# Optimization experiments

Measured on AMD Instinct MI355X. Metric: run time of the kernel, lower is better.

## Reference

```python
import jax, jax.numpy as jnp
import numpy as np

PRUNE_N = 2  # entries zeroed per group
PRUNE_M = 4  # group size along feature dim


def _prune_2of4(x_flat):
    # x_flat: [N, D]; zero out the PRUNE_N smallest-|.| entries in every
    # contiguous group of PRUNE_M columns (matches torch topk(largest=False)
    # + scatter mask semantics, deterministic sort-order tie-breaking).
    N, D = x_flat.shape
    g = x_flat.reshape(N, D // PRUNE_M, PRUNE_M)           # [N, G, 4]
    a = jnp.abs(g)
    order = jnp.argsort(a, axis=-1)                         # ascending |.|
    rank = jnp.argsort(order, axis=-1)                      # rank of each slot
    keep = rank >= PRUNE_N                                  # keep 2 largest
    return jnp.where(keep, g, jnp.zeros_like(g)).reshape(N, D)


def setup_inputs() -> dict:
    key = jax.random.key(0)
    k1, k2 = jax.random.split(key)
    B, S, D_IN, D_OUT = 2, 4096, 4096, 4096
    x = jax.random.normal(k1, (B, S, D_IN), dtype=jnp.float32)
    weight = jax.random.normal(k2, (D_OUT, D_IN), dtype=jnp.float32) * 0.02
    return {"x": x, "weight": weight}


def reference(x, weight):
    B, S, D = x.shape
    x_flat = x.reshape(B * S, D)
    x_sp = _prune_2of4(x_flat)                              # [B*S, D]
    out = x_sp @ weight.T                                   # [B*S, D_out]
    return out
```

## Files before the change

### kernel.cpp

```cpp
#include <hip/hip_runtime.h>
#include <hip/hip_bf16.h>

typedef float f32x4 __attribute__((ext_vector_type(4)));
typedef __bf16 bf16x8 __attribute__((ext_vector_type(8)));
typedef unsigned short ushort_t;
typedef ushort_t u16x8 __attribute__((ext_vector_type(8)));

__device__ inline ushort_t f2bf_rne(float f) {
  unsigned u = __builtin_bit_cast(unsigned, f);
  unsigned r = (u + 0x7fffu + ((u >> 16) & 1u)) >> 16;
  return (ushort_t)r;
}

__global__ void prune_cast_kernel(const float* __restrict__ x,
                                  ushort_t* __restrict__ xsp, long n8) {
  long i = (long)blockIdx.x * blockDim.x + threadIdx.x;
  if (i >= n8) return;
  const float4* p = reinterpret_cast<const float4*>(x);
  float4 g0 = p[2 * i];
  float4 g1 = p[2 * i + 1];
  float v[8] = {g0.x, g0.y, g0.z, g0.w, g1.x, g1.y, g1.z, g1.w};
  u16x8 o;
#pragma unroll
  for (int g = 0; g < 2; ++g) {
    float a[4];
#pragma unroll
    for (int j = 0; j < 4; ++j) a[j] = fabsf(v[g * 4 + j]);
#pragma unroll
    for (int j = 0; j < 4; ++j) {
      int rank = 0;
#pragma unroll
      for (int k = 0; k < 4; ++k) {
        if (k == j) continue;
        rank += (a[k] < a[j]) || (a[k] == a[j] && k < j);
      }
      o[g * 4 + j] = (rank >= 2) ? f2bf_rne(v[g * 4 + j]) : (ushort_t)0;
    }
  }
  reinterpret_cast<u16x8*>(xsp)[i] = o;
}

__global__ void cast_bf16_kernel(const float* __restrict__ w,
                                 ushort_t* __restrict__ wb, long n8) {
  long i = (long)blockIdx.x * blockDim.x + threadIdx.x;
  if (i >= n8) return;
  const float4* p = reinterpret_cast<const float4*>(w);
  float4 g0 = p[2 * i];
  float4 g1 = p[2 * i + 1];
  u16x8 o;
  o[0] = f2bf_rne(g0.x); o[1] = f2bf_rne(g0.y);
  o[2] = f2bf_rne(g0.z); o[3] = f2bf_rne(g0.w);
  o[4] = f2bf_rne(g1.x); o[5] = f2bf_rne(g1.y);
  o[6] = f2bf_rne(g1.z); o[7] = f2bf_rne(g1.w);
  reinterpret_cast<u16x8*>(wb)[i] = o;
}

#define BAR() __builtin_amdgcn_s_barrier()
#define WAIT_LGKM0() asm volatile("s_waitcnt lgkmcnt(0)" ::: "memory")
#define WAIT_VM4() asm volatile("s_waitcnt vmcnt(4)" ::: "memory")

#define STAGE_A(t1, h, par)                                                    \
  {                                                                            \
    const ushort_t* g0 =                                                       \
        A + (a_row0 + (h) * 128 + srow) * (long)Kd + (t1) * 64 + scol;         \
    const ushort_t* g1 =                                                       \
        A + (a_row0 + (h) * 128 + srow + 8) * (long)Kd + (t1) * 64 + scol;     \
    ushort_t* l0 = &ldsA[((par) * 2 + (h)) * 8192 + w * 1024];                 \
    __builtin_amdgcn_global_load_lds(                                          \
        (const __attribute__((address_space(1))) void*)g0,                     \
        (__attribute__((address_space(3))) void*)l0, 16, 0, 0);                \
    __builtin_amdgcn_global_load_lds(                                          \
        (const __attribute__((address_space(1))) void*)g1,                     \
        (__attribute__((address_space(3))) void*)(l0 + 512), 16, 0, 0);        \
  }

#define STAGE_B(t1, h, par)                                                    \
  {                                                                            \
    const ushort_t* g0 =                                                       \
        B + (b_row0 + (h) * 128 + srow) * (long)Kd + (t1) * 64 + scol;         \
    const ushort_t* g1 =                                                       \
        B + (b_row0 + (h) * 128 + srow + 8) * (long)Kd + (t1) * 64 + scol;     \
    ushort_t* l0 = &ldsB[((par) * 2 + (h)) * 8192 + w * 1024];                 \
    __builtin_amdgcn_global_load_lds(                                          \
        (const __attribute__((address_space(1))) void*)g0,                     \
        (__attribute__((address_space(3))) void*)l0, 16, 0, 0);                \
    __builtin_amdgcn_global_load_lds(                                          \
        (const __attribute__((address_space(1))) void*)g1,                     \
        (__attribute__((address_space(3))) void*)(l0 + 512), 16, 0, 0);        \
  }

#define LDA_FRAG(dst, par, mi, s)                                              \
  dst = *reinterpret_cast<const bf16x8*>(                                      \
      reinterpret_cast<const char*>(ldsA) + ((par) * 2 + wr) * 16384 +         \
      (mi) * 2048 + ((s) ? roff1 : roff0));

#define LDB_FRAG(dst, par, ni, s)                                              \
  dst = *reinterpret_cast<const bf16x8*>(                                      \
      reinterpret_cast<const char*>(ldsB) + ((par) * 2 + (wc >> 1)) * 16384 +  \
      (wc & 1) * 8192 + (ni) * 2048 + ((s) ? roff1 : roff0));

#define MFMA_Q(MH, NH)                                                         \
  __builtin_amdgcn_s_setprio(1);                                               \
  _Pragma("unroll") for (int s = 0; s < 2; ++s)                                \
  _Pragma("unroll") for (int mi = 0; mi < 4; ++mi)                             \
  _Pragma("unroll") for (int ni = 0; ni < 2; ++ni)                             \
      acc[(MH) * 4 + mi][(NH) * 2 + ni] =                                      \
          __builtin_amdgcn_mfma_f32_16x16x32_bf16(                             \
              af[mi][s], bfr[(NH) * 2 + ni][s],                                \
              acc[(MH) * 4 + mi][(NH) * 2 + ni], 0, 0, 0);                     \
  __builtin_amdgcn_s_setprio(0);

#define KTILE(t, PAR)                                                          \
  {           \
    _Pragma("unroll") for (int mi = 0; mi < 4; ++mi)                           \
    _Pragma("unroll") for (int s = 0; s < 2; ++s)                              \
        LDA_FRAG(af[mi][s], PAR, mi, s)                                        \
    _Pragma("unroll") for (int ni = 0; ni < 2; ++ni)                           \
    _Pragma("unroll") for (int s = 0; s < 2; ++s)                              \
        LDB_FRAG(bfr[ni][s], PAR, ni, s)                                       \
    if ((t) + 1 < NT) STAGE_A((t) + 1, 0, (PAR) ^ 1)                           \
    BAR();                                                                     \
    WAIT_LGKM0();                                                              \
    MFMA_Q(0, 0)                                                               \
    BAR();                                                                     \
                      \
    _Pragma("unroll") for (int ni = 2; ni < 4; ++ni)                           \
    _Pragma("unroll") for (int s = 0; s < 2; ++s)                              \
        LDB_FRAG(bfr[ni][s], PAR, ni, s)                                       \
    if ((t) + 1 < NT) STAGE_A((t) + 1, 1, (PAR) ^ 1)                           \
    BAR();                                                                     \
    WAIT_LGKM0();                                                              \
    MFMA_Q(0, 1)                                                               \
    BAR();                                                                     \
                        \
    _Pragma("unroll") for (int mi = 0; mi < 4; ++mi)                           \
    _Pragma("unroll") for (int s = 0; s < 2; ++s)                              \
        LDA_FRAG(af[mi][s], PAR, 4 + mi, s)                                    \
    if ((t) + 2 < NT) STAGE_B((t) + 2, 0, PAR)                                 \
    BAR();                                                                     \
    WAIT_LGKM0();                                                              \
    MFMA_Q(1, 1)                                                               \
    BAR();                                                                     \
                 \
    if ((t) + 2 < NT) STAGE_B((t) + 2, 1, PAR)                                 \
    BAR();                                                                     \
    MFMA_Q(1, 0)                                                               \
    WAIT_VM4();                                                                \
    BAR();                                                                     \
  }

__global__ __launch_bounds__(512, 1) void gemm256_kernel(
    const ushort_t* __restrict__ A,
    const ushort_t* __restrict__ B,
    float* __restrict__ C,
    int M, int N, int Kd) {
  __shared__ ushort_t ldsA[4 * 8192];
  __shared__ ushort_t ldsB[4 * 8192];

  const int tid = threadIdx.x;
  const int lane = tid & 63;
  const int w = tid >> 6;
  const int wr = w >> 2;
  const int wc = w & 3;

  const int b = blockIdx.x;
  const int wg = (b & 7) * (gridDim.x >> 3) + (b >> 3);
  const int nbn = N / 256;
  const int bm = wg / nbn, bn = wg % nbn;
  const long a_row0 = (long)bm * 256;
  const long b_row0 = (long)bn * 256;
  const int NT = Kd / 64;

  const int srow = w * 16 + (lane >> 3);
  const int scol = (((lane & 7) ^ ((lane >> 3) & 7)) << 3);

  const int rl = lane & 15;
  const int q = lane >> 4;
  const int roff0 = rl * 128 + (((q) ^ (rl & 7)) << 4);
  const int roff1 = rl * 128 + (((q | 4) ^ (rl & 7)) << 4);

  f32x4 acc[8][4];
#pragma unroll
  for (int i = 0; i < 8; ++i)
#pragma unroll
    for (int j = 0; j < 4; ++j) acc[i][j] = f32x4{0.f, 0.f, 0.f, 0.f};

  bf16x8 af[4][2];
  bf16x8 bfr[4][2];

  STAGE_B(0, 0, 0)
  STAGE_B(0, 1, 0)
  STAGE_A(0, 0, 0)
  STAGE_A(0, 1, 0)
  STAGE_B(1, 0, 1)
  STAGE_B(1, 1, 1)
  WAIT_VM4();
  BAR();

  for (int t = 0; t < NT; t += 2) {
    KTILE(t, 0)
    KTILE(t + 1, 1)
  }

  const int orow = (lane >> 4) * 4;
  const int ocol = lane & 15;
#pragma unroll
  for (int mi = 0; mi < 8; ++mi)
#pragma unroll
    for (int ni = 0; ni < 4; ++ni) {
      const long r0 = a_row0 + wr * 128 + mi * 16 + orow;
      const long c0 = b_row0 + wc * 64 + ni * 16 + ocol;
#pragma unroll
      for (int r = 0; r < 4; ++r) C[(r0 + r) * N + c0] = acc[mi][ni][r];
    }
}

extern "C" void kernel_launch(void* const* d_in, const int* in_sizes, int n_in,
                              void* d_out, int out_size, void* d_ws,
                              size_t ws_size, hipStream_t stream) {
  const float* x = (const float*)d_in[0];
  const float* w = (const float*)d_in[1];
  float* out = (float*)d_out;

  const int K = 4096;
  const long M = (long)in_sizes[0] / K;
  const int N = in_sizes[1] / K;

  ushort_t* xsp = (ushort_t*)d_ws;
  ushort_t* wb = xsp + (long)M * K;

  const long n8x = M * K / 8;
  prune_cast_kernel<<<(int)((n8x + 255) / 256), 256, 0, stream>>>(x, xsp, n8x);

  const long n8w = (long)N * K / 8;
  cast_bf16_kernel<<<(int)((n8w + 255) / 256), 256, 0, stream>>>(w, wb, n8w);

  const int nwg = (int)(M / 256) * (N / 256);
  gemm256_kernel<<<nwg, 512, 0, stream>>>(xsp, wb, out, (int)M, N, K);
}
```

Baseline: 283.4 us.

## Restructure GEMM k-loop pipeline with split fragment registers and deeper prefetch

Reworks the inner K-tile schedule of the bf16 GEMM so that A and B are both prefetched two tiles ahead, instead of A one tile ahead and B two. The A and B register fragments are split into separate even/odd and low/high banks, so all B fragments and later A fragments can be loaded earlier. The LDS waits become partial (lgkmcnt 4/8), letting MFMAs start before every LDS read has landed. The intent is to hide global-to-LDS and LDS-to-register latency better, at the cost of more registers and more outstanding memory operations.

```diff
diff --git a/kernel.cpp b/kernel.cpp
--- a/kernel.cpp
+++ b/kernel.cpp
@@ -57,7 +57,10 @@
 
 #define BAR() __builtin_amdgcn_s_barrier()
 #define WAIT_LGKM0() asm volatile("s_waitcnt lgkmcnt(0)" ::: "memory")
-#define WAIT_VM4() asm volatile("s_waitcnt vmcnt(4)" ::: "memory")
+#define WAIT_LGKM4() asm volatile("s_waitcnt lgkmcnt(4)" ::: "memory")
+#define WAIT_LGKM8() asm volatile("s_waitcnt lgkmcnt(8)" ::: "memory")
+#define WAIT_VM8() asm volatile("s_waitcnt vmcnt(8)" ::: "memory")
+#define WAIT_VM0() asm volatile("s_waitcnt vmcnt(0)" ::: "memory")
 
 #define STAGE_A(t1, h, par)                                                    \
   {                                                                            \
@@ -99,53 +102,52 @@
       reinterpret_cast<const char*>(ldsB) + ((par) * 2 + (wc >> 1)) * 16384 +  \
       (wc & 1) * 8192 + (ni) * 2048 + ((s) ? roff1 : roff0));
 
-#define MFMA_Q(MH, NH)                                                         \
+#define MFMA_Q(AF, BF, MH, NH)                                                 \
   __builtin_amdgcn_s_setprio(1);                                               \
   _Pragma("unroll") for (int s = 0; s < 2; ++s)                                \
   _Pragma("unroll") for (int mi = 0; mi < 4; ++mi)                             \
   _Pragma("unroll") for (int ni = 0; ni < 2; ++ni)                             \
       acc[(MH) * 4 + mi][(NH) * 2 + ni] =                                      \
           __builtin_amdgcn_mfma_f32_16x16x32_bf16(                             \
-              af[mi][s], bfr[(NH) * 2 + ni][s],                                \
-              acc[(MH) * 4 + mi][(NH) * 2 + ni], 0, 0, 0);                     \
+              AF[mi][s], BF[ni][s], acc[(MH) * 4 + mi][(NH) * 2 + ni],         \
+              0, 0, 0);                                                        \
   __builtin_amdgcn_s_setprio(0);
 
 #define KTILE(t, PAR)                                                          \
-  {           \
+  {                   \
     _Pragma("unroll") for (int mi = 0; mi < 4; ++mi)                           \
     _Pragma("unroll") for (int s = 0; s < 2; ++s)                              \
-        LDA_FRAG(af[mi][s], PAR, mi, s)                                        \
+        LDA_FRAG(afE[mi][s], PAR, mi, s)                                       \
     _Pragma("unroll") for (int ni = 0; ni < 2; ++ni)                           \
     _Pragma("unroll") for (int s = 0; s < 2; ++s)                              \
-        LDB_FRAG(bfr[ni][s], PAR, ni, s)                                       \
-    if ((t) + 1 < NT) STAGE_A((t) + 1, 0, (PAR) ^ 1)                           \
+        LDB_FRAG(b01[ni][s], PAR, ni, s)                                       \
+    _Pragma("unroll") for (int ni = 0; ni < 2; ++ni)                           \
+    _Pragma("unroll") for (int s = 0; s < 2; ++s)                              \
+        LDB_FRAG(b23[ni][s], PAR, 2 + ni, s)                                   \
+    BAR();                                                                     \
+    WAIT_LGKM4();                                                              \
+    MFMA_Q(afE, b01, 0, 0)                                                     \
+    BAR();                                                                     \
+                     \
+    _Pragma("unroll") for (int mi = 0; mi < 4; ++mi)                           \
+    _Pragma("unroll") for (int s = 0; s < 2; ++s)                              \
+        LDA_FRAG(afO[mi][s], PAR, 4 + mi, s)                                   \
+    if ((t) + 2 < NT) STAGE_A((t) + 2, 0, PAR)                                 \
+    BAR();                                                                     \
+    WAIT_LGKM8();                                                              \
+    MFMA_Q(afE, b23, 0, 1)                                                     \
+    BAR();                                                                     \
+                                      \
+    if ((t) + 2 < NT) { STAGE_B((t) + 2, 0, PAR) STAGE_B((t) + 2, 1, PAR) }    \
     BAR();                                                                     \
     WAIT_LGKM0();                                                              \
-    MFMA_Q(0, 0)                                                               \
-    BAR();                                                                     \
-                      \
-    _Pragma("unroll") for (int ni = 2; ni < 4; ++ni)                           \
-    _Pragma("unroll") for (int s = 0; s < 2; ++s)                              \
-        LDB_FRAG(bfr[ni][s], PAR, ni, s)                                       \
-    if ((t) + 1 < NT) STAGE_A((t) + 1, 1, (PAR) ^ 1)                           \
-    BAR();                                                                     \
-    WAIT_LGKM0();                                                              \
-    MFMA_Q(0, 1)                                                               \
-    BAR();                                                                     \
-                        \
-    _Pragma("unroll") for (int mi = 0; mi < 4; ++mi)                           \
-    _Pragma("unroll") for (int s = 0; s < 2; ++s)                              \
-        LDA_FRAG(af[mi][s], PAR, 4 + mi, s)                                    \
-    if ((t) + 2 < NT) STAGE_B((t) + 2, 0, PAR)                                 \
-    BAR();                                                                     \
-    WAIT_LGKM0();                                                              \
-    MFMA_Q(1, 1)                                                               \
-    BAR();                                                                     \
-                 \
-    if ((t) + 2 < NT) STAGE_B((t) + 2, 1, PAR)                                 \
-    BAR();                                                                     \
-    MFMA_Q(1, 0)                                                               \
-    WAIT_VM4();                                                                \
+    MFMA_Q(afO, b23, 1, 1)                                                     \
+    BAR();                                                                     \
+                         \
+    if ((t) + 2 < NT) STAGE_A((t) + 2, 1, PAR)                                 \
+    BAR();                                                                     \
+    MFMA_Q(afO, b01, 1, 0)                                                     \
+    if ((t) + 2 < NT) { WAIT_VM8(); } else { WAIT_VM0(); }                     \
     BAR();                                                                     \
   }
 
@@ -185,16 +187,20 @@
 #pragma unroll
     for (int j = 0; j < 4; ++j) acc[i][j] = f32x4{0.f, 0.f, 0.f, 0.f};
 
-  bf16x8 af[4][2];
-  bf16x8 bfr[4][2];
-
+  bf16x8 afE[4][2];
+  bf16x8 afO[4][2];
+  bf16x8 b01[2][2];
+  bf16x8 b23[2][2];
+
+  STAGE_A(0, 0, 0)
+  STAGE_A(0, 1, 0)
   STAGE_B(0, 0, 0)
   STAGE_B(0, 1, 0)
-  STAGE_A(0, 0, 0)
-  STAGE_A(0, 1, 0)
+  STAGE_A(1, 0, 1)
+  STAGE_A(1, 1, 1)
   STAGE_B(1, 0, 1)
   STAGE_B(1, 1, 1)
-  WAIT_VM4();
+  WAIT_VM8();
   BAR();
 
   for (int t = 0; t < NT; t += 2) {
```

Result: slower. 491.8 us (+73.5%).

## Cut per-tile barriers from eight to two and stage loads unconditionally

Applied to the files above, without the earlier changes.

Restructures the GEMM K-tile loop so each tile uses two barriers instead of eight, with no explicit LDS waits. All B fragments are loaded up front and the A/B stage loads are issued in larger batches. Stage indices are clamped at the tail instead of branched, and a final vmcnt(0) drain is added before the epilogue. The aim is to cut barrier stalls and let MFMA overlap more with LDS and global loads. The risks are weaker LDS read/write ordering, since redundant tail loads could overwrite buffers still being read, and higher register pressure.

```diff
diff --git a/kernel.cpp b/kernel.cpp
--- a/kernel.cpp
+++ b/kernel.cpp
@@ -55,9 +55,12 @@
   reinterpret_cast<u16x8*>(wb)[i] = o;
 }
 
-#define BAR() __builtin_amdgcn_s_barrier()
-#define WAIT_LGKM0() asm volatile("s_waitcnt lgkmcnt(0)" ::: "memory")
+#define BARM()                              \
+  asm volatile("" ::: "memory");            \
+  __builtin_amdgcn_s_barrier();             \
+  asm volatile("" ::: "memory");
 #define WAIT_VM4() asm volatile("s_waitcnt vmcnt(4)" ::: "memory")
+#define WAIT_VM0() asm volatile("s_waitcnt vmcnt(0)" ::: "memory")
 
 #define STAGE_A(t1, h, par)                                                    \
   {                                                                            \
@@ -111,42 +114,31 @@
   __builtin_amdgcn_s_setprio(0);
 
 #define KTILE(t, PAR)                                                          \
-  {           \
+  {                                                                            \
+    const int tA = ((t) + 1 < NT) ? (t) + 1 : NT - 1;                          \
+    const int tB = ((t) + 2 < NT) ? (t) + 2 : NT - 1;                          \
+            \
     _Pragma("unroll") for (int mi = 0; mi < 4; ++mi)                           \
     _Pragma("unroll") for (int s = 0; s < 2; ++s)                              \
         LDA_FRAG(af[mi][s], PAR, mi, s)                                        \
-    _Pragma("unroll") for (int ni = 0; ni < 2; ++ni)                           \
+    _Pragma("unroll") for (int ni = 0; ni < 4; ++ni)                           \
     _Pragma("unroll") for (int s = 0; s < 2; ++s)                              \
         LDB_FRAG(bfr[ni][s], PAR, ni, s)                                       \
-    if ((t) + 1 < NT) STAGE_A((t) + 1, 0, (PAR) ^ 1)                           \
-    BAR();                                                                     \
-    WAIT_LGKM0();                                                              \
+    STAGE_A(tA, 0, (PAR) ^ 1)                                                  \
+    STAGE_A(tA, 1, (PAR) ^ 1)                                                  \
     MFMA_Q(0, 0)                                                               \
-    BAR();                                                                     \
-                      \
-    _Pragma("unroll") for (int ni = 2; ni < 4; ++ni)                           \
-    _Pragma("unroll") for (int s = 0; s < 2; ++s)                              \
-        LDB_FRAG(bfr[ni][s], PAR, ni, s)                                       \
-    if ((t) + 1 < NT) STAGE_A((t) + 1, 1, (PAR) ^ 1)                           \
-    BAR();                                                                     \
-    WAIT_LGKM0();                                                              \
     MFMA_Q(0, 1)                                                               \
-    BAR();                                                                     \
-                        \
     _Pragma("unroll") for (int mi = 0; mi < 4; ++mi)                           \
     _Pragma("unroll") for (int s = 0; s < 2; ++s)                              \
         LDA_FRAG(af[mi][s], PAR, 4 + mi, s)                                    \
-    if ((t) + 2 < NT) STAGE_B((t) + 2, 0, PAR)                                 \
-    BAR();                                                                     \
-    WAIT_LGKM0();                                                              \
     MFMA_Q(1, 1)                                                               \
-    BAR();                                                                     \
-                 \
-    if ((t) + 2 < NT) STAGE_B((t) + 2, 1, PAR)                                 \
-    BAR();                                                                     \
+                     \
+    BARM()                                                                     \
+    STAGE_B(tB, 0, PAR)                                                        \
+    STAGE_B(tB, 1, PAR)                                                        \
     MFMA_Q(1, 0)                                                               \
     WAIT_VM4();                                                                \
-    BAR();                                                                     \
+    BARM()                                                                     \
   }
 
 __global__ __launch_bounds__(512, 1) void gemm256_kernel(
@@ -188,19 +180,20 @@
   bf16x8 af[4][2];
   bf16x8 bfr[4][2];
 
+  STAGE_A(0, 0, 0)
+  STAGE_A(0, 1, 0)
   STAGE_B(0, 0, 0)
   STAGE_B(0, 1, 0)
-  STAGE_A(0, 0, 0)
-  STAGE_A(0, 1, 0)
   STAGE_B(1, 0, 1)
   STAGE_B(1, 1, 1)
   WAIT_VM4();
-  BAR();
+  BARM()
 
   for (int t = 0; t < NT; t += 2) {
     KTILE(t, 0)
     KTILE(t + 1, 1)
   }
+  WAIT_VM0();
 
   const int orow = (lane >> 4) * 4;
   const int ocol = lane & 15;
```

New measurement: 267.4 us. 5.6% less time.
